# Optimization experiments

Hardware: AMD Instinct MI355X
Metric: run time of the kernel (lower is better)

Reference implementation:

```python
import jax, jax.numpy as jnp
import numpy as np

KEY_DIM = 32
D = 128  # attn_ratio * key_dim
H = 8
DIM = 512
N = 1024
B = 16
EPS = 1e-5


def setup_inputs() -> dict:
    key = jax.random.key(0)
    ks = jax.random.split(key, 5)
    x = jax.random.normal(ks[0], (B, DIM, N), dtype=jnp.float32)
    # grouped Conv1d(dim -> H*(2*key_dim+d), k=1, groups=H): per-group weight [H, 192, 64]
    qkv_w = jax.random.normal(ks[1], (H, 2 * KEY_DIM + D, DIM // H), dtype=jnp.float32) * 0.05
    qkv_b = jax.random.normal(ks[2], (H, 2 * KEY_DIM + D), dtype=jnp.float32) * 0.02
    # proj Conv1d(d*H -> dim, k=1)
    proj_w = jax.random.normal(ks[3], (DIM, D * H), dtype=jnp.float32) * 0.03
    proj_b = jax.random.normal(ks[4], (DIM,), dtype=jnp.float32) * 0.02
    bn_gamma = jnp.ones((DIM,), dtype=jnp.float32)
    bn_beta = jnp.zeros((DIM,), dtype=jnp.float32)
    bn_mean = jnp.zeros((DIM,), dtype=jnp.float32)
    bn_var = jnp.ones((DIM,), dtype=jnp.float32)
    return {"x": x, "qkv_w": qkv_w, "qkv_b": qkv_b, "proj_w": proj_w,
            "proj_b": proj_b, "bn_gamma": bn_gamma, "bn_beta": bn_beta,
            "bn_mean": bn_mean, "bn_var": bn_var}


def reference(x, qkv_w, qkv_b, proj_w, proj_b, bn_gamma, bn_beta, bn_mean, bn_var):
    Bx, C, Nx = x.shape
    scale = KEY_DIM ** (-0.5)
    # grouped 1x1 conv: split channels into H groups of C//H
    xh = x.reshape(Bx, H, C // H, Nx)                      # [B,H,Cg,N]
    qkv = jnp.einsum('bhcn,hoc->bhon', xh, qkv_w) + qkv_b[None, :, :, None]
    q, k, v = jnp.split(qkv, [KEY_DIM, 2 * KEY_DIM], axis=2)  # [B,H,kd,N],[B,H,kd,N],[B,H,d,N]
    # attn[m,n] = sum_c q[c,m]*k[c,n]
    attn = jnp.einsum('bhcm,bhcn->bhmn', q, k) * scale      # [B,H,N,N]
    attn = jax.nn.softmax(attn, axis=-1)
    # out[d,m] = sum_n v[d,n]*attn[m,n]  (v @ attn^T)
    o = jnp.einsum('bhdn,bhmn->bhdm', v, attn)              # [B,H,d,N]
    o = o.reshape(Bx, H * D, Nx)
    # proj: ReLU -> 1x1 conv -> BatchNorm1d (inference mode)
    o = jax.nn.relu(o)
    o = jnp.einsum('bcn,oc->bon', o, proj_w) + proj_b[None, :, None]
    inv = bn_gamma / jnp.sqrt(bn_var + EPS)
    o = o * inv[None, :, None] + (bn_beta - bn_mean * inv)[None, :, None]
    return o
```

## Files before the change

### kernel.cpp

```cpp
#include <hip/hip_runtime.h>
#include <math.h>

typedef unsigned short u16;
typedef unsigned int u32;

#define Bb   16
#define Hh   8
#define KD   32
#define DV   128
#define DIM  512
#define Nn   1024
#define OQKV 192
#define SCALE 0.17677669529663687f

typedef short bf16x8 __attribute__((ext_vector_type(8)));
typedef float f32x16 __attribute__((ext_vector_type(16)));

#define MFMA32(a, b, c) __builtin_amdgcn_mfma_f32_32x32x16_bf16(a, b, c, 0, 0, 0)

__device__ __forceinline__ u16 f2bf_rn(float f) {
  return (u16)((__float_as_uint(f) + 0x8000u) >> 16);
}
__device__ __forceinline__ u32 pkrn(float lo, float hi) {
  u32 a = __float_as_uint(lo) + 0x8000u;
  u32 b = __float_as_uint(hi) + 0x8000u;
  return __builtin_amdgcn_perm(b, a, 0x07060302);
}

__global__ __launch_bounds__(256) void qkv_kernel(
    const float* __restrict__ x, const float* __restrict__ w,
    const float* __restrict__ bias, u16* __restrict__ Qb,
    u16* __restrict__ Kb, u16* __restrict__ Vb) {
  const int nt = blockIdx.x, bh = blockIdx.y;
  const int b = bh >> 3, h = bh & 7;
  const int tid = threadIdx.x;
  const int wid = tid >> 6, lane = tid & 63;
  const int r32 = lane & 31, hh = lane >> 5;
  const int n0 = nt * 128;

  __shared__ __align__(16) u16 Ws[192 * 72];
  __shared__ __align__(16) u16 Xs[128 * 72];

  const float* wp = w + (size_t)h * OQKV * 64;
  #pragma unroll
  for (int i = 0; i < 12; ++i) {
    int idx = i * 256 + tid;
    int o = idx >> 4, c4 = (idx & 15) * 4;
    float4 wv = *(const float4*)&wp[o * 64 + c4];
    uint2 pk; pk.x = pkrn(wv.x, wv.y); pk.y = pkrn(wv.z, wv.w);
    *(uint2*)&Ws[o * 72 + c4] = pk;
  }
  const float* xp = x + ((size_t)b * DIM + h * 64) * Nn + n0;
  #pragma unroll
  for (int i = 0; i < 8; ++i) {
    int idx = i * 256 + tid;
    int c = idx >> 5, n4 = (idx & 31) * 4;
    float4 xv = *(const float4*)&xp[(size_t)c * Nn + n4];
    Xs[(n4 + 0) * 72 + c] = f2bf_rn(xv.x);
    Xs[(n4 + 1) * 72 + c] = f2bf_rn(xv.y);
    Xs[(n4 + 2) * 72 + c] = f2bf_rn(xv.z);
    Xs[(n4 + 3) * 72 + c] = f2bf_rn(xv.w);
  }
  __syncthreads();

  f32x16 acc[6];
  #pragma unroll
  for (int t = 0; t < 6; ++t)
    #pragma unroll
    for (int r = 0; r < 16; ++r) acc[t][r] = 0.0f;

  const int nw = wid * 32;
  #pragma unroll
  for (int k = 0; k < 4; ++k) {
    const int ko = k * 16 + hh * 8;
    bf16x8 xb = *(const bf16x8*)&Xs[(nw + r32) * 72 + ko];
    #pragma unroll
    for (int t = 0; t < 6; ++t) {
      bf16x8 wa = *(const bf16x8*)&Ws[(t * 32 + r32) * 72 + ko];
      acc[t] = MFMA32(wa, xb, acc[t]);
    }
  }

  const int n = n0 + nw + r32;
  const float* bp = bias + h * OQKV;
  #pragma unroll
  for (int t = 0; t < 6; ++t) {
    #pragma unroll
    for (int g = 0; g < 4; ++g) {
      const int ob = t * 32 + 8 * g + 4 * hh;
      float4 bv = *(const float4*)&bp[ob];
      float v0 = acc[t][4 * g + 0] + bv.x;
      float v1 = acc[t][4 * g + 1] + bv.y;
      float v2 = acc[t][4 * g + 2] + bv.z;
      float v3 = acc[t][4 * g + 3] + bv.w;
      if (t == 0) {
        uint2 pk;
        pk.x = pkrn(v0 * SCALE, v1 * SCALE);
        pk.y = pkrn(v2 * SCALE, v3 * SCALE);
        *(uint2*)&Qb[((size_t)bh * Nn + n) * 32 + ob] = pk;
      } else if (t == 1) {
        uint2 pk; pk.x = pkrn(v0, v1); pk.y = pkrn(v2, v3);
        *(uint2*)&Kb[((size_t)bh * Nn + n) * 32 + ob - 32] = pk;
      } else {
        const int d = ob - 64;
        Vb[((size_t)bh * DV + d + 0) * Nn + n] = f2bf_rn(v0);
        Vb[((size_t)bh * DV + d + 1) * Nn + n] = f2bf_rn(v1);
        Vb[((size_t)bh * DV + d + 2) * Nn + n] = f2bf_rn(v2);
        Vb[((size_t)bh * DV + d + 3) * Nn + n] = f2bf_rn(v3);
      }
    }
  }
}

__global__ __launch_bounds__(256) void attn_kernel(
    const u16* __restrict__ Qb, const u16* __restrict__ Kb,
    const u16* __restrict__ Vb, u16* __restrict__ Ot) {
  const int mt = blockIdx.x, bh = blockIdx.y;
  const int b = bh >> 3, h = bh & 7;
  const int tid = threadIdx.x;
  const int wid = tid >> 6, lane = tid & 63;
  const int r32 = lane & 31, hh = lane >> 5;
  const int m0 = mt * 128;

  __shared__ __align__(16) u16 Vc[128 * 40];

  const u16* qp = Qb + ((size_t)bh * Nn + m0 + wid * 32 + r32) * 32;
  const bf16x8 qb0 = *(const bf16x8*)&qp[hh * 8];
  const bf16x8 qb1 = *(const bf16x8*)&qp[16 + hh * 8];

  const u16* kbase = Kb + (size_t)bh * Nn * 32;
  const u16* vbase = Vb + (size_t)bh * DV * Nn;

  f32x16 o[4];
  #pragma unroll
  for (int t = 0; t < 4; ++t)
    #pragma unroll
    for (int r = 0; r < 16; ++r) o[t][r] = 0.0f;
  float lsum = 0.0f;

  for (int ch = 0; ch < Nn / 32; ++ch) {
    const int n0 = ch * 32;
    __syncthreads();

    #pragma unroll
    for (int i = 0; i < 2; ++i) {
      int idx = i * 256 + tid;
      int d = idx >> 2, n8 = (idx & 3) * 8;
      *(uint4*)&Vc[d * 40 + n8] = *(const uint4*)&vbase[(size_t)d * Nn + n0 + n8];
    }
    __syncthreads();

    const u16* kp = kbase + (size_t)(n0 + r32) * 32;
    bf16x8 ka0 = *(const bf16x8*)&kp[hh * 8];
    bf16x8 ka1 = *(const bf16x8*)&kp[16 + hh * 8];

    f32x16 s;
    #pragma unroll
    for (int r = 0; r < 16; ++r) s[r] = 0.0f;
    s = MFMA32(ka0, qb0, s);
    s = MFMA32(ka1, qb1, s);

    float csum = 0.0f;
    #pragma unroll
    for (int r = 0; r < 16; ++r) { s[r] = __expf(s[r]); csum += s[r]; }
    lsum += csum;

    u32 Pk[8], Rk[8];
    #pragma unroll
    for (int g = 0; g < 4; ++g) {
      Pk[2 * g]     = pkrn(s[4 * g + 0], s[4 * g + 1]);
      Pk[2 * g + 1] = pkrn(s[4 * g + 2], s[4 * g + 3]);
    }
    #pragma unroll
    for (int i = 0; i < 8; ++i) Rk[i] = __shfl_xor(Pk[i], 32, 64);

    union { u32 d[4]; bf16x8 v; } pb0u, pb1u;
    pb0u.d[0] = hh ? Rk[2] : Pk[0];
    pb0u.d[1] = hh ? Rk[3] : Pk[1];
    pb0u.d[2] = hh ? Pk[2] : Rk[0];
    pb0u.d[3] = hh ? Pk[3] : Rk[1];
    pb1u.d[0] = hh ? Rk[6] : Pk[4];
    pb1u.d[1] = hh ? Rk[7] : Pk[5];
    pb1u.d[2] = hh ? Pk[6] : Rk[4];
    pb1u.d[3] = hh ? Pk[7] : Rk[5];

    #pragma unroll
    for (int t = 0; t < 4; ++t) {
      bf16x8 va0 = *(const bf16x8*)&Vc[(t * 32 + r32) * 40 + hh * 8];
      bf16x8 va1 = *(const bf16x8*)&Vc[(t * 32 + r32) * 40 + 16 + hh * 8];
      o[t] = MFMA32(va0, pb0u.v, o[t]);
      o[t] = MFMA32(va1, pb1u.v, o[t]);
    }
  }

  lsum += __shfl_xor(lsum, 32, 64);
  const float inv = 1.0f / lsum;
  const int m = m0 + wid * 32 + r32;
  u16* obase = Ot + ((size_t)b * Nn + m) * 1024 + h * DV + 4 * hh;
  #pragma unroll
  for (int t = 0; t < 4; ++t) {
    #pragma unroll
    for (int g = 0; g < 4; ++g) {
      float v0 = fmaxf(o[t][4 * g + 0] * inv, 0.0f);
      float v1 = fmaxf(o[t][4 * g + 1] * inv, 0.0f);
      float v2 = fmaxf(o[t][4 * g + 2] * inv, 0.0f);
      float v3 = fmaxf(o[t][4 * g + 3] * inv, 0.0f);
      uint2 pk; pk.x = pkrn(v0, v1); pk.y = pkrn(v2, v3);
      *(uint2*)&obase[t * 32 + 8 * g] = pk;
    }
  }
}

__global__ __launch_bounds__(256) void proj_kernel(
    const u16* __restrict__ Ot, const float* __restrict__ pw,
    const float* __restrict__ pb, const float* __restrict__ bn_g,
    const float* __restrict__ bn_b, const float* __restrict__ bn_m,
    const float* __restrict__ bn_v, float* __restrict__ out) {
  const int n0 = blockIdx.x * 128, oc0 = blockIdx.y * 128, b = blockIdx.z;
  const int tid = threadIdx.x;
  const int wid = tid >> 6, lane = tid & 63;
  const int r32 = lane & 31, hh = lane >> 5;
  const int ocw = (wid >> 1) * 64, nw = (wid & 1) * 64;

  __shared__ __align__(16) u16 Ws[128 * 40];
  __shared__ __align__(16) u16 Os[128 * 40];

  f32x16 o[2][2];
  #pragma unroll
  for (int t = 0; t < 2; ++t)
    #pragma unroll
    for (int u = 0; u < 2; ++u)
      #pragma unroll
      for (int r = 0; r < 16; ++r) o[t][u][r] = 0.0f;

  for (int ic0 = 0; ic0 < 1024; ic0 += 32) {
    __syncthreads();
    #pragma unroll
    for (int i = 0; i < 4; ++i) {
      int idx = i * 256 + tid;
      int row = idx >> 3, icq = (idx & 7) * 4;
      float4 wv = *(const float4*)&pw[(size_t)(oc0 + row) * 1024 + ic0 + icq];
      uint2 pk; pk.x = pkrn(wv.x, wv.y); pk.y = pkrn(wv.z, wv.w);
      *(uint2*)&Ws[row * 40 + icq] = pk;
    }
    #pragma unroll
    for (int i = 0; i < 2; ++i) {
      int idx = i * 256 + tid;
      int row = idx >> 2, ic8 = (idx & 3) * 8;
      *(uint4*)&Os[row * 40 + ic8] =
          *(const uint4*)&Ot[((size_t)b * Nn + n0 + row) * 1024 + ic0 + ic8];
    }
    __syncthreads();

    #pragma unroll
    for (int s = 0; s < 2; ++s) {
      const int ko = s * 16 + hh * 8;
      bf16x8 a0 = *(const bf16x8*)&Ws[(ocw + r32) * 40 + ko];
      bf16x8 a1 = *(const bf16x8*)&Ws[(ocw + 32 + r32) * 40 + ko];
      bf16x8 b0 = *(const bf16x8*)&Os[(nw + r32) * 40 + ko];
      bf16x8 b1 = *(const bf16x8*)&Os[(nw + 32 + r32) * 40 + ko];
      o[0][0] = MFMA32(a0, b0, o[0][0]);
      o[0][1] = MFMA32(a0, b1, o[0][1]);
      o[1][0] = MFMA32(a1, b0, o[1][0]);
      o[1][1] = MFMA32(a1, b1, o[1][1]);
    }
  }

  #pragma unroll
  for (int t = 0; t < 2; ++t) {
    const int obase = oc0 + ocw + t * 32 + 4 * hh;
    #pragma unroll
    for (int g = 0; g < 4; ++g) {
      const int oc = obase + 8 * g;
      float4 gv = *(const float4*)&bn_g[oc];
      float4 vv = *(const float4*)&bn_v[oc];
      float4 bv = *(const float4*)&bn_b[oc];
      float4 mv = *(const float4*)&bn_m[oc];
      float4 pv = *(const float4*)&pb[oc];
      float inv4[4], add4[4];
      inv4[0] = gv.x * rsqrtf(vv.x + 1e-5f);
      inv4[1] = gv.y * rsqrtf(vv.y + 1e-5f);
      inv4[2] = gv.z * rsqrtf(vv.z + 1e-5f);
      inv4[3] = gv.w * rsqrtf(vv.w + 1e-5f);
      add4[0] = pv.x * inv4[0] + bv.x - mv.x * inv4[0];
      add4[1] = pv.y * inv4[1] + bv.y - mv.y * inv4[1];
      add4[2] = pv.z * inv4[2] + bv.z - mv.z * inv4[2];
      add4[3] = pv.w * inv4[3] + bv.w - mv.w * inv4[3];
      #pragma unroll
      for (int u = 0; u < 2; ++u) {
        const int n = n0 + nw + u * 32 + r32;
        #pragma unroll
        for (int i = 0; i < 4; ++i) {
          float val = o[t][u][4 * g + i] * inv4[i] + add4[i];
          out[((size_t)b * DIM + oc + i) * Nn + n] = val;
        }
      }
    }
  }
}

extern "C" void kernel_launch(void* const* d_in, const int* in_sizes, int n_in,
                              void* d_out, int out_size, void* d_ws,
                              size_t ws_size, hipStream_t stream) {
  const float* x      = (const float*)d_in[0];
  const float* qkv_w  = (const float*)d_in[1];
  const float* qkv_b  = (const float*)d_in[2];
  const float* proj_w = (const float*)d_in[3];
  const float* proj_b = (const float*)d_in[4];
  const float* bn_g   = (const float*)d_in[5];
  const float* bn_b   = (const float*)d_in[6];
  const float* bn_m   = (const float*)d_in[7];
  const float* bn_v   = (const float*)d_in[8];
  float* out = (float*)d_out;

  char* ws = (char*)d_ws;
  u16* Qb = (u16*)(ws);
  u16* Kb = (u16*)(ws + 8388608);
  u16* Vb = (u16*)(ws + 16777216);
  u16* Ot = (u16*)(ws + 50331648);

  qkv_kernel<<<dim3(8, Bb * Hh), 256, 0, stream>>>(x, qkv_w, qkv_b, Qb, Kb, Vb);
  attn_kernel<<<dim3(8, Bb * Hh), 256, 0, stream>>>(Qb, Kb, Vb, Ot);
  proj_kernel<<<dim3(8, 4, Bb), 256, 0, stream>>>(
      Ot, proj_w, proj_b, bn_g, bn_b, bn_m, bn_v, out);
}
```

Before: 225.9 us.

## Read V directly from global in attention, swap MFMA roles, transpose output layout

The attention kernel no longer stages V chunks through shared memory with two barriers per iteration. Each wave now reads V rows straight from global/L2 and swaps the MFMA operand order so the output is channel-major. The output is written in a [B, C, N] layout, and the projection kernel transposes it while loading into shared memory. Other changes: exp is replaced by exp2 with log2(e) folded into the Q scale, and blocks are remapped so each XCD handles contiguous heads for L2 locality. The costs are redundant global V reads across waves and scattered 2-byte LDS stores in the projection kernel.

```diff
diff --git a/kernel.cpp b/kernel.cpp
--- a/kernel.cpp
+++ b/kernel.cpp
@@ -11,12 +11,20 @@
 #define DIM  512
 #define Nn   1024
 #define OQKV 192
-#define SCALE 0.17677669529663687f
+#define SCALE2 0.25503490221320355f
 
 typedef short bf16x8 __attribute__((ext_vector_type(8)));
 typedef float f32x16 __attribute__((ext_vector_type(16)));
 
 #define MFMA32(a, b, c) __builtin_amdgcn_mfma_f32_32x32x16_bf16(a, b, c, 0, 0, 0)
+
+__device__ __forceinline__ float fexp2(float x) {
+#if __has_builtin(__builtin_amdgcn_exp2f)
+  return __builtin_amdgcn_exp2f(x);
+#else
+  return exp2f(x);
+#endif
+}
 
 __device__ __forceinline__ u16 f2bf_rn(float f) {
   return (u16)((__float_as_uint(f) + 0x8000u) >> 16);
@@ -95,8 +103,8 @@
       float v3 = acc[t][4 * g + 3] + bv.w;
       if (t == 0) {
         uint2 pk;
-        pk.x = pkrn(v0 * SCALE, v1 * SCALE);
-        pk.y = pkrn(v2 * SCALE, v3 * SCALE);
+        pk.x = pkrn(v0 * SCALE2, v1 * SCALE2);
+        pk.y = pkrn(v2 * SCALE2, v3 * SCALE2);
         *(uint2*)&Qb[((size_t)bh * Nn + n) * 32 + ob] = pk;
       } else if (t == 1) {
         uint2 pk; pk.x = pkrn(v0, v1); pk.y = pkrn(v2, v3);
@@ -114,17 +122,19 @@
 
 __global__ __launch_bounds__(256) void attn_kernel(
     const u16* __restrict__ Qb, const u16* __restrict__ Kb,
-    const u16* __restrict__ Vb, u16* __restrict__ Ot) {
-  const int mt = blockIdx.x, bh = blockIdx.y;
-  const int b = bh >> 3, h = bh & 7;
+    const u16* __restrict__ Vb, u16* __restrict__ Ot2) {
+  const int blk = blockIdx.x;
+  const int xcd = blk & 7, j = blk >> 3;
+  const int bh = (xcd << 4) | (j >> 3);
+  const int mt = j & 7;
   const int tid = threadIdx.x;
   const int wid = tid >> 6, lane = tid & 63;
   const int r32 = lane & 31, hh = lane >> 5;
-  const int m0 = mt * 128;
-
-  __shared__ __align__(16) u16 Vc[128 * 40];
-
-  const u16* qp = Qb + ((size_t)bh * Nn + m0 + wid * 32 + r32) * 32;
+  const int mw = mt * 128 + wid * 32;
+
+  __shared__ float Lw[4][32];
+
+  const u16* qp = Qb + ((size_t)bh * Nn + mw + r32) * 32;
   const bf16x8 qb0 = *(const bf16x8*)&qp[hh * 8];
   const bf16x8 qb1 = *(const bf16x8*)&qp[16 + hh * 8];
 
@@ -140,15 +150,6 @@
 
   for (int ch = 0; ch < Nn / 32; ++ch) {
     const int n0 = ch * 32;
-    __syncthreads();
-
-    #pragma unroll
-    for (int i = 0; i < 2; ++i) {
-      int idx = i * 256 + tid;
-      int d = idx >> 2, n8 = (idx & 3) * 8;
-      *(uint4*)&Vc[d * 40 + n8] = *(const uint4*)&vbase[(size_t)d * Nn + n0 + n8];
-    }
-    __syncthreads();
 
     const u16* kp = kbase + (size_t)(n0 + r32) * 32;
     bf16x8 ka0 = *(const bf16x8*)&kp[hh * 8];
@@ -162,7 +163,7 @@
 
     float csum = 0.0f;
     #pragma unroll
-    for (int r = 0; r < 16; ++r) { s[r] = __expf(s[r]); csum += s[r]; }
+    for (int r = 0; r < 16; ++r) { s[r] = fexp2(s[r]); csum += s[r]; }
     lsum += csum;
 
     u32 Pk[8], Rk[8];
@@ -174,45 +175,49 @@
     #pragma unroll
     for (int i = 0; i < 8; ++i) Rk[i] = __shfl_xor(Pk[i], 32, 64);
 
-    union { u32 d[4]; bf16x8 v; } pb0u, pb1u;
-    pb0u.d[0] = hh ? Rk[2] : Pk[0];
-    pb0u.d[1] = hh ? Rk[3] : Pk[1];
-    pb0u.d[2] = hh ? Pk[2] : Rk[0];
-    pb0u.d[3] = hh ? Pk[3] : Rk[1];
-    pb1u.d[0] = hh ? Rk[6] : Pk[4];
-    pb1u.d[1] = hh ? Rk[7] : Pk[5];
-    pb1u.d[2] = hh ? Pk[6] : Rk[4];
-    pb1u.d[3] = hh ? Pk[7] : Rk[5];
-
+    union { u32 d[4]; bf16x8 v; } pa0, pa1;
+    pa0.d[0] = hh ? Rk[2] : Pk[0];
+    pa0.d[1] = hh ? Rk[3] : Pk[1];
+    pa0.d[2] = hh ? Pk[2] : Rk[0];
+    pa0.d[3] = hh ? Pk[3] : Rk[1];
+    pa1.d[0] = hh ? Rk[6] : Pk[4];
+    pa1.d[1] = hh ? Rk[7] : Pk[5];
+    pa1.d[2] = hh ? Pk[6] : Rk[4];
+    pa1.d[3] = hh ? Pk[7] : Rk[5];
+
+    const u16* vp = vbase + n0;
     #pragma unroll
     for (int t = 0; t < 4; ++t) {
-      bf16x8 va0 = *(const bf16x8*)&Vc[(t * 32 + r32) * 40 + hh * 8];
-      bf16x8 va1 = *(const bf16x8*)&Vc[(t * 32 + r32) * 40 + 16 + hh * 8];
-      o[t] = MFMA32(va0, pb0u.v, o[t]);
-      o[t] = MFMA32(va1, pb1u.v, o[t]);
+      const u16* vr = vp + (size_t)(t * 32 + r32) * Nn;
+      bf16x8 vb0 = *(const bf16x8*)&vr[hh * 8];
+      bf16x8 vb1 = *(const bf16x8*)&vr[16 + hh * 8];
+      o[t] = MFMA32(pa0.v, vb0, o[t]);
+      o[t] = MFMA32(pa1.v, vb1, o[t]);
     }
   }
 
   lsum += __shfl_xor(lsum, 32, 64);
-  const float inv = 1.0f / lsum;
-  const int m = m0 + wid * 32 + r32;
-  u16* obase = Ot + ((size_t)b * Nn + m) * 1024 + h * DV + 4 * hh;
+  Lw[wid][r32] = 1.0f / lsum;
+  asm volatile("s_waitcnt lgkmcnt(0)" ::: "memory");
+
   #pragma unroll
   for (int t = 0; t < 4; ++t) {
+    u16* orow = Ot2 + ((size_t)bh * DV + t * 32 + r32) * Nn;
     #pragma unroll
     for (int g = 0; g < 4; ++g) {
-      float v0 = fmaxf(o[t][4 * g + 0] * inv, 0.0f);
-      float v1 = fmaxf(o[t][4 * g + 1] * inv, 0.0f);
-      float v2 = fmaxf(o[t][4 * g + 2] * inv, 0.0f);
-      float v3 = fmaxf(o[t][4 * g + 3] * inv, 0.0f);
+      float4 iv = *(const float4*)&Lw[wid][8 * g + 4 * hh];
+      float v0 = fmaxf(o[t][4 * g + 0] * iv.x, 0.0f);
+      float v1 = fmaxf(o[t][4 * g + 1] * iv.y, 0.0f);
+      float v2 = fmaxf(o[t][4 * g + 2] * iv.z, 0.0f);
+      float v3 = fmaxf(o[t][4 * g + 3] * iv.w, 0.0f);
       uint2 pk; pk.x = pkrn(v0, v1); pk.y = pkrn(v2, v3);
-      *(uint2*)&obase[t * 32 + 8 * g] = pk;
+      *(uint2*)&orow[mw + 8 * g + 4 * hh] = pk;
     }
   }
 }
 
 __global__ __launch_bounds__(256) void proj_kernel(
-    const u16* __restrict__ Ot, const float* __restrict__ pw,
+    const u16* __restrict__ Ot2, const float* __restrict__ pw,
     const float* __restrict__ pb, const float* __restrict__ bn_g,
     const float* __restrict__ bn_b, const float* __restrict__ bn_m,
     const float* __restrict__ bn_v, float* __restrict__ out) {
@@ -246,9 +251,12 @@
     #pragma unroll
     for (int i = 0; i < 2; ++i) {
       int idx = i * 256 + tid;
-      int row = idx >> 2, ic8 = (idx & 3) * 8;
-      *(uint4*)&Os[row * 40 + ic8] =
-          *(const uint4*)&Ot[((size_t)b * Nn + n0 + row) * 1024 + ic0 + ic8];
+      int ic = idx >> 4, n8 = (idx & 15) * 8;
+      uint4 ov = *(const uint4*)
+          &Ot2[((size_t)b * 1024 + ic0 + ic) * Nn + n0 + n8];
+      const u16* op = (const u16*)&ov;
+      #pragma unroll
+      for (int jj = 0; jj < 8; ++jj) Os[(n8 + jj) * 40 + ic] = op[jj];
     }
     __syncthreads();
 
@@ -314,13 +322,13 @@
   float* out = (float*)d_out;
 
   char* ws = (char*)d_ws;
-  u16* Qb = (u16*)(ws);
-  u16* Kb = (u16*)(ws + 8388608);
-  u16* Vb = (u16*)(ws + 16777216);
-  u16* Ot = (u16*)(ws + 50331648);
+  u16* Qb  = (u16*)(ws);
+  u16* Kb  = (u16*)(ws + 8388608);
+  u16* Vb  = (u16*)(ws + 16777216);
+  u16* Ot2 = (u16*)(ws + 50331648);
 
   qkv_kernel<<<dim3(8, Bb * Hh), 256, 0, stream>>>(x, qkv_w, qkv_b, Qb, Kb, Vb);
-  attn_kernel<<<dim3(8, Bb * Hh), 256, 0, stream>>>(Qb, Kb, Vb, Ot);
+  attn_kernel<<<dim3(1024), 256, 0, stream>>>(Qb, Kb, Vb, Ot2);
   proj_kernel<<<dim3(8, 4, Bb), 256, 0, stream>>>(
-      Ot, proj_w, proj_b, bn_g, bn_b, bn_m, bn_v, out);
-}
+      Ot2, proj_w, proj_b, bn_g, bn_b, bn_m, bn_v, out);
+}
```

Result: slower. 320.2 us (+41.7%).

## Double-buffer V tiles, widen attention chunks, use exp2, and remap blocks per XCD

Applied to the files above, without the earlier changes.

The attention kernel now processes 64 keys per iteration and double-buffers the V tile in shared memory. It prefetches the next tile into registers while computing, which cuts the syncthreads per iteration from two to one. The softmax uses exp2 with log2(e) folded into the Q scale. Both attention and projection launches switch to 1D grids whose block index is remapped so that blocks sharing a batch/head land on the same XCD for L2 reuse. The trade-offs are higher register and LDS use, which may lower occupancy.

```diff
diff --git a/kernel.cpp b/kernel.cpp
--- a/kernel.cpp
+++ b/kernel.cpp
@@ -11,12 +11,20 @@
 #define DIM  512
 #define Nn   1024
 #define OQKV 192
-#define SCALE 0.17677669529663687f
+#define SCALE2 0.25503490221320355f
 
 typedef short bf16x8 __attribute__((ext_vector_type(8)));
 typedef float f32x16 __attribute__((ext_vector_type(16)));
 
 #define MFMA32(a, b, c) __builtin_amdgcn_mfma_f32_32x32x16_bf16(a, b, c, 0, 0, 0)
+
+__device__ __forceinline__ float fexp2(float x) {
+#if __has_builtin(__builtin_amdgcn_exp2f)
+  return __builtin_amdgcn_exp2f(x);
+#else
+  return exp2f(x);
+#endif
+}
 
 __device__ __forceinline__ u16 f2bf_rn(float f) {
   return (u16)((__float_as_uint(f) + 0x8000u) >> 16);
@@ -95,8 +103,8 @@
       float v3 = acc[t][4 * g + 3] + bv.w;
       if (t == 0) {
         uint2 pk;
-        pk.x = pkrn(v0 * SCALE, v1 * SCALE);
-        pk.y = pkrn(v2 * SCALE, v3 * SCALE);
+        pk.x = pkrn(v0 * SCALE2, v1 * SCALE2);
+        pk.y = pkrn(v2 * SCALE2, v3 * SCALE2);
         *(uint2*)&Qb[((size_t)bh * Nn + n) * 32 + ob] = pk;
       } else if (t == 1) {
         uint2 pk; pk.x = pkrn(v0, v1); pk.y = pkrn(v2, v3);
@@ -115,22 +123,39 @@
 __global__ __launch_bounds__(256) void attn_kernel(
     const u16* __restrict__ Qb, const u16* __restrict__ Kb,
     const u16* __restrict__ Vb, u16* __restrict__ Ot) {
-  const int mt = blockIdx.x, bh = blockIdx.y;
-  const int b = bh >> 3, h = bh & 7;
+  const int blk = blockIdx.x;
+  const int xcd = blk & 7, j = blk >> 3;
+  const int bh = (xcd << 4) | (j >> 3);
+  const int mt = j & 7;
   const int tid = threadIdx.x;
   const int wid = tid >> 6, lane = tid & 63;
   const int r32 = lane & 31, hh = lane >> 5;
-  const int m0 = mt * 128;
-
-  __shared__ __align__(16) u16 Vc[128 * 40];
-
-  const u16* qp = Qb + ((size_t)bh * Nn + m0 + wid * 32 + r32) * 32;
+  const int mw = mt * 128 + wid * 32;
+
+  __shared__ __align__(16) u16 Vs[2][128 * 72];
+
+  const u16* qp = Qb + ((size_t)bh * Nn + mw + r32) * 32;
   const bf16x8 qb0 = *(const bf16x8*)&qp[hh * 8];
   const bf16x8 qb1 = *(const bf16x8*)&qp[16 + hh * 8];
 
   const u16* kbase = Kb + (size_t)bh * Nn * 32;
   const u16* vbase = Vb + (size_t)bh * DV * Nn;
 
+  int sd[4], sn[4];
+  #pragma unroll
+  for (int i = 0; i < 4; ++i) {
+    int idx = i * 256 + tid;
+    sd[i] = idx >> 3; sn[i] = (idx & 7) * 8;
+  }
+
+  uint4 vreg[4];
+  #pragma unroll
+  for (int i = 0; i < 4; ++i)
+    vreg[i] = *(const uint4*)&vbase[(size_t)sd[i] * Nn + sn[i]];
+  #pragma unroll
+  for (int i = 0; i < 4; ++i)
+    *(uint4*)&Vs[0][sd[i] * 72 + sn[i]] = vreg[i];
+
   f32x16 o[4];
   #pragma unroll
   for (int t = 0; t < 4; ++t)
@@ -138,64 +163,85 @@
     for (int r = 0; r < 16; ++r) o[t][r] = 0.0f;
   float lsum = 0.0f;
 
-  for (int ch = 0; ch < Nn / 32; ++ch) {
-    const int n0 = ch * 32;
+  for (int ch = 0; ch < 16; ++ch) {
+    const int n0 = ch * 64;
+    const int p = ch & 1;
     __syncthreads();
 
-    #pragma unroll
-    for (int i = 0; i < 2; ++i) {
-      int idx = i * 256 + tid;
-      int d = idx >> 2, n8 = (idx & 3) * 8;
-      *(uint4*)&Vc[d * 40 + n8] = *(const uint4*)&vbase[(size_t)d * Nn + n0 + n8];
-    }
-    __syncthreads();
-
-    const u16* kp = kbase + (size_t)(n0 + r32) * 32;
-    bf16x8 ka0 = *(const bf16x8*)&kp[hh * 8];
-    bf16x8 ka1 = *(const bf16x8*)&kp[16 + hh * 8];
-
-    f32x16 s;
-    #pragma unroll
-    for (int r = 0; r < 16; ++r) s[r] = 0.0f;
-    s = MFMA32(ka0, qb0, s);
-    s = MFMA32(ka1, qb1, s);
+    if (ch < 15) {
+      #pragma unroll
+      for (int i = 0; i < 4; ++i)
+        vreg[i] = *(const uint4*)&vbase[(size_t)sd[i] * Nn + n0 + 64 + sn[i]];
+    }
+
+    const u16* kp0 = kbase + (size_t)(n0 + r32) * 32;
+    const u16* kp1 = kbase + (size_t)(n0 + 32 + r32) * 32;
+    bf16x8 ka0 = *(const bf16x8*)&kp0[hh * 8];
+    bf16x8 ka1 = *(const bf16x8*)&kp0[16 + hh * 8];
+    bf16x8 ka2 = *(const bf16x8*)&kp1[hh * 8];
+    bf16x8 ka3 = *(const bf16x8*)&kp1[16 + hh * 8];
+
+    f32x16 c0, c1;
+    #pragma unroll
+    for (int r = 0; r < 16; ++r) { c0[r] = 0.0f; c1[r] = 0.0f; }
+    c0 = MFMA32(ka0, qb0, c0);
+    c0 = MFMA32(ka1, qb1, c0);
+    c1 = MFMA32(ka2, qb0, c1);
+    c1 = MFMA32(ka3, qb1, c1);
 
     float csum = 0.0f;
     #pragma unroll
-    for (int r = 0; r < 16; ++r) { s[r] = __expf(s[r]); csum += s[r]; }
+    for (int r = 0; r < 16; ++r) { c0[r] = fexp2(c0[r]); csum += c0[r]; }
+    #pragma unroll
+    for (int r = 0; r < 16; ++r) { c1[r] = fexp2(c1[r]); csum += c1[r]; }
     lsum += csum;
 
-    u32 Pk[8], Rk[8];
+    u32 Pk[16], Rk[16];
     #pragma unroll
     for (int g = 0; g < 4; ++g) {
-      Pk[2 * g]     = pkrn(s[4 * g + 0], s[4 * g + 1]);
-      Pk[2 * g + 1] = pkrn(s[4 * g + 2], s[4 * g + 3]);
-    }
-    #pragma unroll
-    for (int i = 0; i < 8; ++i) Rk[i] = __shfl_xor(Pk[i], 32, 64);
-
-    union { u32 d[4]; bf16x8 v; } pb0u, pb1u;
-    pb0u.d[0] = hh ? Rk[2] : Pk[0];
-    pb0u.d[1] = hh ? Rk[3] : Pk[1];
-    pb0u.d[2] = hh ? Pk[2] : Rk[0];
-    pb0u.d[3] = hh ? Pk[3] : Rk[1];
-    pb1u.d[0] = hh ? Rk[6] : Pk[4];
-    pb1u.d[1] = hh ? Rk[7] : Pk[5];
-    pb1u.d[2] = hh ? Pk[6] : Rk[4];
-    pb1u.d[3] = hh ? Pk[7] : Rk[5];
+      Pk[2 * g]     = pkrn(c0[4 * g + 0], c0[4 * g + 1]);
+      Pk[2 * g + 1] = pkrn(c0[4 * g + 2], c0[4 * g + 3]);
+      Pk[8 + 2 * g]     = pkrn(c1[4 * g + 0], c1[4 * g + 1]);
+      Pk[8 + 2 * g + 1] = pkrn(c1[4 * g + 2], c1[4 * g + 3]);
+    }
+    #pragma unroll
+    for (int i = 0; i < 16; ++i) Rk[i] = __shfl_xor(Pk[i], 32, 64);
+
+    union { u32 d[4]; bf16x8 v; } pb[4];
+    #pragma unroll
+    for (int q = 0; q < 2; ++q) {
+      const int base = 8 * q;
+      pb[2 * q].d[0] = hh ? Rk[base + 2] : Pk[base + 0];
+      pb[2 * q].d[1] = hh ? Rk[base + 3] : Pk[base + 1];
+      pb[2 * q].d[2] = hh ? Pk[base + 2] : Rk[base + 0];
+      pb[2 * q].d[3] = hh ? Pk[base + 3] : Rk[base + 1];
+      pb[2 * q + 1].d[0] = hh ? Rk[base + 6] : Pk[base + 4];
+      pb[2 * q + 1].d[1] = hh ? Rk[base + 7] : Pk[base + 5];
+      pb[2 * q + 1].d[2] = hh ? Pk[base + 6] : Rk[base + 4];
+      pb[2 * q + 1].d[3] = hh ? Pk[base + 7] : Rk[base + 5];
+    }
 
     #pragma unroll
     for (int t = 0; t < 4; ++t) {
-      bf16x8 va0 = *(const bf16x8*)&Vc[(t * 32 + r32) * 40 + hh * 8];
-      bf16x8 va1 = *(const bf16x8*)&Vc[(t * 32 + r32) * 40 + 16 + hh * 8];
-      o[t] = MFMA32(va0, pb0u.v, o[t]);
-      o[t] = MFMA32(va1, pb1u.v, o[t]);
+      const u16* vrow = &Vs[p][(t * 32 + r32) * 72];
+      #pragma unroll
+      for (int s = 0; s < 4; ++s) {
+        bf16x8 va = *(const bf16x8*)&vrow[s * 16 + hh * 8];
+        o[t] = MFMA32(va, pb[s].v, o[t]);
+      }
+    }
+
+    if (ch < 15) {
+      #pragma unroll
+      for (int i = 0; i < 4; ++i)
+        *(uint4*)&Vs[1 - p][sd[i] * 72 + sn[i]] = vreg[i];
     }
   }
 
   lsum += __shfl_xor(lsum, 32, 64);
   const float inv = 1.0f / lsum;
-  const int m = m0 + wid * 32 + r32;
+  const int m = mw + r32;
+  const int b = bh >> 3, h = bh & 7;
   u16* obase = Ot + ((size_t)b * Nn + m) * 1024 + h * DV + 4 * hh;
   #pragma unroll
   for (int t = 0; t < 4; ++t) {
@@ -216,7 +262,12 @@
     const float* __restrict__ pb, const float* __restrict__ bn_g,
     const float* __restrict__ bn_b, const float* __restrict__ bn_m,
     const float* __restrict__ bn_v, float* __restrict__ out) {
-  const int n0 = blockIdx.x * 128, oc0 = blockIdx.y * 128, b = blockIdx.z;
+  const int blk = blockIdx.x;
+  const int xcd = blk & 7, rr = blk >> 3;
+  const int pairl = rr >> 2, oct = rr & 3;
+  const int pair = xcd * 16 + pairl;
+  const int b = pair >> 3, nt = pair & 7;
+  const int n0 = nt * 128, oc0 = oct * 128;
   const int tid = threadIdx.x;
   const int wid = tid >> 6, lane = tid & 63;
   const int r32 = lane & 31, hh = lane >> 5;
@@ -320,7 +371,7 @@
   u16* Ot = (u16*)(ws + 50331648);
 
   qkv_kernel<<<dim3(8, Bb * Hh), 256, 0, stream>>>(x, qkv_w, qkv_b, Qb, Kb, Vb);
-  attn_kernel<<<dim3(8, Bb * Hh), 256, 0, stream>>>(Qb, Kb, Vb, Ot);
-  proj_kernel<<<dim3(8, 4, Bb), 256, 0, stream>>>(
+  attn_kernel<<<dim3(1024), 256, 0, stream>>>(Qb, Kb, Vb, Ot);
+  proj_kernel<<<dim3(512), 256, 0, stream>>>(
       Ot, proj_w, proj_b, bn_g, bn_b, bn_m, bn_v, out);
 }
```

New measurement: 220.3 us. 2.5% less time.
